# Kernel tuning notes

Measured on AMD Instinct MI355X. Metric: run time of the kernel, lower is better.

## Reference

```python
import jax, jax.numpy as jnp
import numpy as np

N = 51200      # total nodes
G = 256        # graphs in batch
NPG = 200      # nodes per graph
E = 409600     # intra-graph edges
EPG = E // G
F_IN, HID, HEADS, NCLS = 768, 128, 4, 2


def setup_inputs() -> dict:
    key = jax.random.key(0)
    ks = jax.random.split(key, 20)
    x = jax.random.normal(ks[0], (N, F_IN), jnp.float32)
    # edges strictly inside each graph, no self-loops (PyG batching semantics)
    gid = jnp.arange(E, dtype=jnp.int32) // EPG
    sl = jax.random.randint(ks[1], (E,), 0, NPG, dtype=jnp.int32)
    off = jax.random.randint(ks[2], (E,), 1, NPG, dtype=jnp.int32)
    dl = (sl + off) % NPG
    edge_index = jnp.stack([gid * NPG + sl, gid * NPG + dl])
    batch = jnp.arange(N, dtype=jnp.int32) // NPG

    def glorot(k, shape, fan_in):
        return jax.random.normal(k, shape, jnp.float32) * np.float32(1.0 / np.sqrt(fan_in))

    return {
        'x': x, 'edge_index': edge_index, 'batch': batch,
        'W1': glorot(ks[3], (F_IN, HEADS * HID), F_IN),
        'a_src1': glorot(ks[4], (HEADS, HID), HID),
        'a_dst1': glorot(ks[5], (HEADS, HID), HID),
        'b1': jnp.zeros((HEADS * HID,), jnp.float32),
        'W2': glorot(ks[6], (HEADS * HID, HID), HEADS * HID),
        'a_src2': glorot(ks[7], (1, HID), HID),
        'a_dst2': glorot(ks[8], (1, HID), HID),
        'b2': jnp.zeros((HID,), jnp.float32),
        'Wc': glorot(ks[9], (HID, 2), HID),
        'bc': jnp.zeros((2,), jnp.float32),
        'Wf1': glorot(ks[10], (HID, HID), HID),
        'bf1': jnp.zeros((HID,), jnp.float32),
        'Wf2': glorot(ks[11], (HID, NCLS), HID),
        'bf2': jnp.zeros((NCLS,), jnp.float32),
    }


def _segment_softmax(logits, seg, num):
    m = jax.ops.segment_max(logits, seg, num_segments=num)
    e = jnp.exp(logits - m[seg])
    s = jax.ops.segment_sum(e, seg, num_segments=num)
    return e / (s[seg] + 1e-16)


def _gat(x, src, dst, W, a_s, a_d, b, n):
    # PyG GATConv, eval mode (attention dropout off), self-loops already in src/dst
    H, C = a_s.shape
    h = (x @ W).reshape(n, H, C)                       # [n,H,C]
    a_src = (h * a_s).sum(-1)                          # [n,H]
    a_dst = (h * a_d).sum(-1)
    logits = jax.nn.leaky_relu(a_src[src] + a_dst[dst], 0.2)  # [Etot,H]
    alpha = _segment_softmax(logits, dst, n)
    out = jax.ops.segment_sum(h[src] * alpha[:, :, None], dst, num_segments=n)
    return out.reshape(n, H * C) + b


def reference(x, edge_index, batch, W1, a_src1, a_dst1, b1, W2, a_src2, a_dst2, b2,
              Wc, bc, Wf1, bf1, Wf2, bf2):
    src0, dst0 = edge_index[0], edge_index[1]
    loop = jnp.arange(N, dtype=src0.dtype)
    src = jnp.concatenate([src0, loop])
    dst = jnp.concatenate([dst0, loop])

    h1 = jax.nn.relu(_gat(x, src, dst, W1, a_src1, a_dst1, b1, N))     # [N,512]
    h2 = jax.nn.relu(_gat(h1, src, dst, W2, a_src2, a_dst2, b2, N))    # [N,128]

    S = jax.nn.softmax(h2 @ Wc + bc, axis=1)                           # [N,2]

    # aggregate(): per-graph S^T A S via per-edge outer products (A from original edges)
    eg = batch[src0]
    outer = S[src0][:, :, None] * S[dst0][:, None, :]                  # [E,2,2]
    agg = jax.ops.segment_sum(outer, eg, num_segments=G)               # [G,2,2]
    rnorm = jnp.clip(jnp.abs(agg).sum(axis=2, keepdims=True), 1e-5, None)  # F.normalize p=1 dim=1
    nadj = agg / rnorm
    diag = jnp.diagonal(nadj, axis1=1, axis2=2)                        # [G,2]
    aggregate_loss = jnp.mean(jnp.mean((diag - 1.0) ** 2, axis=1))     # MSE vs ones, averaged over graphs

    # subgraph embedding: first row of S_g^T x_g per graph
    sub = jax.ops.segment_sum(S[:, 0:1] * h2, batch, num_segments=G)   # [G,128]

    out = jax.nn.relu(sub @ Wf1 + bf1)                                 # eval: dropout off
    out = out @ Wf2 + bf2                                              # [G,2]
    return out, aggregate_loss
```

## Files before the change

kernel.cpp:

```cpp
#include <hip/hip_runtime.h>
#include <hip/hip_bf16.h>
#include <cstdint>

#define N_NODES 51200
#define N_GRAPH 256
#define NPG     200
#define N_EDGE  409600
#define EPG     1600
#define F_IN    768
#define HID     128
#define HEADS   4
#define HC      512

typedef __attribute__((ext_vector_type(8))) short short8;
typedef __attribute__((ext_vector_type(4))) float floatx4;

constexpr size_t OFF_H1B    = 0;
constexpr size_t OFF_H2B    = OFF_H1B + (size_t)N_NODES * HC * 2;
constexpr size_t OFF_H2F    = OFF_H2B + (size_t)N_NODES * HID * 2;
constexpr size_t OFF_WT1    = OFF_H2F + (size_t)N_NODES * HID * 4;
constexpr size_t OFF_WT2    = OFF_WT1 + (size_t)HC * F_IN * 2;
constexpr size_t OFF_S      = OFF_WT2 + (size_t)HID * HC * 2;
constexpr size_t OFF_AGG    = OFF_S + (size_t)N_NODES * 2 * 4;
constexpr size_t OFF_SUB    = OFF_AGG + (size_t)N_GRAPH * 4 * 4;
constexpr size_t OFF_EORD   = OFF_SUB + (size_t)N_GRAPH * HID * 4;
constexpr size_t OFF_ROWS   = OFF_EORD + (size_t)N_GRAPH * EPG * 2;

__device__ __forceinline__ float leaky(float x) { return x >= 0.0f ? x : 0.2f * x; }

__device__ __forceinline__ unsigned short f2bf(float f) {
    unsigned int u = __float_as_uint(f);
    u += 0x7fffu + ((u >> 16) & 1u);
    return (unsigned short)(u >> 16);
}
__device__ __forceinline__ float bflo(int p) { return __uint_as_float((unsigned)p << 16); }
__device__ __forceinline__ float bfhi(int p) { return __uint_as_float((unsigned)p & 0xffff0000u); }

__device__ __forceinline__ unsigned int cvtpk(float lo, float hi) {
    unsigned int r;
    asm("v_cvt_pk_bf16_f32 %0, %1, %2" : "=v"(r) : "v"(lo), "v"(hi));
    return r;
}

__device__ __forceinline__ void gl_lds16(const void* g, void* l) {
    __builtin_amdgcn_global_load_lds(
        (__attribute__((address_space(1))) void*)(g),
        (__attribute__((address_space(3))) void*)(l),
        16, 0, 0);
}

__global__ __launch_bounds__(256)
void transpose_cvt_kernel(const float* __restrict__ W, short* __restrict__ Wt,
                          int K, int Nn)
{
    int idx = blockIdx.x * 256 + threadIdx.x;
    if (idx >= K * Nn) return;
    int k = idx / Nn, n = idx % Nn;
    Wt[(size_t)n * K + k] = (short)f2bf(W[idx]);
}

__global__ __launch_bounds__(512, 2)
void gemm_xw1_kernel(const float* __restrict__ A, const short* __restrict__ Bt,
                     unsigned short* __restrict__ C, int M, int Nn, int K)
{
    __shared__ __align__(16) float Asm[3][256 * 32];
    __shared__ __align__(16) short Bsm[3][256 * 32];
    const int tid = threadIdx.x;
    const int w = tid >> 6, l = tid & 63;

    const int nwg = gridDim.x;
    int wg = blockIdx.x;
    wg = (wg & 7) * (nwg >> 3) + (wg >> 3);
    const int nbx = Nn >> 8;
    const int m0 = (wg / nbx) * 256;
    const int n0 = (wg % nbx) * 256;
    const int wr = w >> 2, wc = w & 3;

    floatx4 acc[8][4];
#pragma unroll
    for (int i = 0; i < 8; ++i)
#pragma unroll
        for (int j = 0; j < 4; ++j) acc[i][j] = (floatx4)0.0f;

    const short* bgp = Bt + (size_t)(n0 + w * 32 + (l & 15)) * K + ((l >> 4) * 8);
    const float* agp = A + (size_t)(m0 + w * 32 + (l & 7)) * K + ((l >> 3) * 4);
    const int nt = K >> 5;

    int aB[8];
#pragma unroll
    for (int mi = 0; mi < 8; ++mi) {
        const int r = wr * 128 + mi * 16 + (l & 15);
        aB[mi] = (r >> 3) * 256 + (l >> 4) * 64 + (r & 7) * 4;
    }
    const int bB0 = wc * 2048 + l * 8;

#define STAGEX(buf, t) {                                                        \
        const int ko_ = (t) * 32;                                               \
        gl_lds16(agp + ko_,              &Asm[buf][(w * 4 + 0) * 256]);         \
        gl_lds16(agp + 8 * K + ko_,      &Asm[buf][(w * 4 + 1) * 256]);         \
        gl_lds16(agp + 16 * K + ko_,     &Asm[buf][(w * 4 + 2) * 256]);         \
        gl_lds16(agp + 24 * K + ko_,     &Asm[buf][(w * 4 + 3) * 256]);         \
        gl_lds16(bgp + ko_,              &Bsm[buf][w * 1024]);                  \
        gl_lds16(bgp + 16 * K + ko_,     &Bsm[buf][w * 1024 + 512]); }

#define COMPUTEX(buf) {                                                         \
        short8 bfr[4];                                                          \
        _Pragma("unroll")                                                       \
        for (int ni = 0; ni < 4; ++ni)                                          \
            bfr[ni] = *(const short8*)&Bsm[buf][bB0 + ni * 512];                \
        _Pragma("unroll")                                                       \
        for (int mh = 0; mh < 2; ++mh) {                                        \
            short8 af[4];                                                       \
            _Pragma("unroll")                                                   \
            for (int q = 0; q < 4; ++q) {                                       \
                float4 v0 = *(const float4*)&Asm[buf][aB[mh * 4 + q]];          \
                float4 v1 = *(const float4*)&Asm[buf][aB[mh * 4 + q] + 32];     \
                uint4 pk;                                                       \
                pk.x = cvtpk(v0.x, v0.y); pk.y = cvtpk(v0.z, v0.w);             \
                pk.z = cvtpk(v1.x, v1.y); pk.w = cvtpk(v1.z, v1.w);             \
                af[q] = *reinterpret_cast<short8*>(&pk);                        \
            }                                                                   \
            _Pragma("unroll")                                                   \
            for (int q = 0; q < 4; ++q)                                         \
                _Pragma("unroll")                                               \
                for (int ni = 0; ni < 4; ++ni)                                  \
                    acc[mh * 4 + q][ni] = __builtin_amdgcn_mfma_f32_16x16x32_bf16( \
                        af[q], bfr[ni], acc[mh * 4 + q][ni], 0, 0, 0);          \
        } }

    STAGEX(0, 0);
    STAGEX(1, 1);
    asm volatile("s_waitcnt vmcnt(6)" ::: "memory");
    __builtin_amdgcn_s_barrier();

    int cur3 = 0;
    for (int t = 0; t < nt; ++t) {
        int nn3 = cur3 + 2; if (nn3 >= 3) nn3 -= 3;
        if (t + 2 < nt) STAGEX(nn3, t + 2);
        COMPUTEX(cur3);
        if (t + 1 < nt) {
            if (t + 2 < nt) asm volatile("s_waitcnt vmcnt(6) lgkmcnt(0)" ::: "memory");
            else            asm volatile("s_waitcnt vmcnt(0) lgkmcnt(0)" ::: "memory");
            __builtin_amdgcn_s_barrier();
        }
        cur3 += 1; if (cur3 == 3) cur3 = 0;
    }
#undef STAGEX
#undef COMPUTEX

    const int lr = (l >> 4) * 4, lc = l & 15;
#pragma unroll
    for (int mi = 0; mi < 8; ++mi)
#pragma unroll
        for (int ni = 0; ni < 4; ++ni) {
            const size_t base = (size_t)(m0 + wr * 128 + mi * 16 + lr) * Nn
                              + (n0 + wc * 64 + ni * 16 + lc);
#pragma unroll
            for (int rr = 0; rr < 4; ++rr)
                C[base + (size_t)rr * Nn] = f2bf(acc[mi][ni][rr]);
        }
}

__global__ __launch_bounds__(256)
void gemm_bf16_kernel(const short* __restrict__ Ab, const short* __restrict__ Bt,
                      unsigned short* __restrict__ C, int M, int Nn, int K)
{
    __shared__ __align__(16) short Bblob[3][4096];
    __shared__ __align__(16) short Ablob[3][4096];
    const int tid = threadIdx.x;
    const int w = tid >> 6, l = tid & 63;

    const int nwg = gridDim.x;
    int wg = blockIdx.x;
    wg = (wg & 7) * (nwg >> 3) + (wg >> 3);
    const int nbx = Nn >> 7;
    const int m0 = (wg / nbx) * 128;
    const int n0 = (wg % nbx) * 128;
    const int wr = w >> 1, wc = w & 1;
    const int wofs = w * 1024;

    floatx4 acc[4][4];
#pragma unroll
    for (int i = 0; i < 4; ++i)
#pragma unroll
        for (int j = 0; j < 4; ++j) acc[i][j] = (floatx4)0.0f;

    const short* bgp = Bt + (size_t)(n0 + w * 32 + (l & 15)) * K + ((l >> 4) * 8);
    const short* agp = Ab + (size_t)(m0 + w * 32 + (l & 15)) * K + ((l >> 4) * 8);
    const int nt = K >> 5;

    auto compute = [&](int bi) {
        short8 af[4], bfr[4];
#pragma unroll
        for (int mi = 0; mi < 4; ++mi)
            af[mi] = *(const short8*)&Ablob[bi][(wr * 4 + mi) * 512 + l * 8];
#pragma unroll
        for (int ni = 0; ni < 4; ++ni)
            bfr[ni] = *(const short8*)&Bblob[bi][(wc * 4 + ni) * 512 + l * 8];
#pragma unroll
        for (int mi = 0; mi < 4; ++mi)
#pragma unroll
            for (int ni = 0; ni < 4; ++ni)
                acc[mi][ni] = __builtin_amdgcn_mfma_f32_16x16x32_bf16(
                    af[mi], bfr[ni], acc[mi][ni], 0, 0, 0);
    };

    gl_lds16(agp,               &Ablob[0][wofs]);
    gl_lds16(agp + 16 * K,      &Ablob[0][wofs + 512]);
    gl_lds16(bgp,               &Bblob[0][wofs]);
    gl_lds16(bgp + 16 * K,      &Bblob[0][wofs + 512]);
    gl_lds16(agp + 32,          &Ablob[1][wofs]);
    gl_lds16(agp + 16 * K + 32, &Ablob[1][wofs + 512]);
    gl_lds16(bgp + 32,          &Bblob[1][wofs]);
    gl_lds16(bgp + 16 * K + 32, &Bblob[1][wofs + 512]);
    asm volatile("s_waitcnt vmcnt(4)" ::: "memory");
    __builtin_amdgcn_s_barrier();

    int cur3 = 0;
    for (int t = 0; t < nt; ++t) {
        int nn3 = cur3 + 2; if (nn3 >= 3) nn3 -= 3;
        if (t + 2 < nt) {
            const int kk = (t + 2) << 5;
            gl_lds16(agp + kk,          &Ablob[nn3][wofs]);
            gl_lds16(agp + 16 * K + kk, &Ablob[nn3][wofs + 512]);
            gl_lds16(bgp + kk,          &Bblob[nn3][wofs]);
            gl_lds16(bgp + 16 * K + kk, &Bblob[nn3][wofs + 512]);
        }
        compute(cur3);
        if (t + 1 < nt) {
            if (t + 2 < nt) asm volatile("s_waitcnt vmcnt(4) lgkmcnt(0)" ::: "memory");
            else            asm volatile("s_waitcnt vmcnt(0) lgkmcnt(0)" ::: "memory");
            __builtin_amdgcn_s_barrier();
        }
        cur3 += 1; if (cur3 == 3) cur3 = 0;
    }

    const int lr = (l >> 4) * 4, lc = l & 15;
#pragma unroll
    for (int mi = 0; mi < 4; ++mi)
#pragma unroll
        for (int ni = 0; ni < 4; ++ni) {
            const size_t base = (size_t)(m0 + wr * 64 + mi * 16 + lr) * Nn
                              + (n0 + wc * 64 + ni * 16 + lc);
#pragma unroll
            for (int rr = 0; rr < 4; ++rr)
                C[base + (size_t)rr * Nn] = f2bf(acc[mi][ni][rr]);
        }
}

__global__ __launch_bounds__(256)
void csr_kernel(const int* __restrict__ src0, const int* __restrict__ dst0,
                unsigned short* __restrict__ eord, int* __restrict__ rows)
{
    const int g = blockIdx.x, tid = threadIdx.x;
    __shared__ unsigned short s_eraw[EPG];
    __shared__ int s_cnt[NPG];
    __shared__ int s_scan[256];
    __shared__ int s_row[NPG + 1];
    const int gbase = g * NPG;

    if (tid < NPG) s_cnt[tid] = 0;
    for (int j = tid; j < EPG; j += 256) {
        int s = src0[g * EPG + j] - gbase;
        int d = dst0[g * EPG + j] - gbase;
        s_eraw[j] = (unsigned short)(s | (d << 8));
    }
    __syncthreads();
    for (int j = tid; j < EPG; j += 256)
        atomicAdd(&s_cnt[s_eraw[j] >> 8], 1);
    __syncthreads();
    {
        int v = (tid < NPG) ? s_cnt[tid] : 0;
        s_scan[tid] = v;
        __syncthreads();
        for (int off = 1; off < 256; off <<= 1) {
            int u = (tid >= off) ? s_scan[tid - off] : 0;
            __syncthreads();
            s_scan[tid] += u;
            __syncthreads();
        }
        if (tid < NPG) s_row[tid + 1] = s_scan[tid];
        if (tid == 0) s_row[0] = 0;
        __syncthreads();
        if (tid < NPG) s_scan[tid] = s_row[tid];
    }
    __syncthreads();
    for (int j = tid; j < EPG; j += 256) {
        int pk = s_eraw[j];
        int p = atomicAdd(&s_scan[pk >> 8], 1);
        eord[(size_t)g * EPG + p] = (unsigned short)pk;
    }
    if (tid <= NPG) rows[g * (NPG + 1) + tid] = s_row[tid];
}

__global__ __launch_bounds__(512)
void gat1_kernel(const unsigned short* __restrict__ H,
                 const unsigned short* __restrict__ eord, const int* __restrict__ rows,
                 const float* __restrict__ a_s, const float* __restrict__ a_d,
                 const float* __restrict__ b1, unsigned short* __restrict__ out)
{
    const int g = blockIdx.x, h = blockIdx.y;
    __shared__ int   s_feat[NPG * 64];
    __shared__ float s_as[NPG], s_ad[NPG], s_m[NPG], s_inv[NPG];
    __shared__ int   s_row[NPG + 1];
    __shared__ int2  s_wc[EPG];
    const int tid = threadIdx.x, w = tid >> 6, l = tid & 63;
    const int gbase = g * NPG;

    for (int flat = tid; flat < NPG * 16; flat += 512) {
        int row = flat >> 4, q = flat & 15;
        uint4 v = *(const uint4*)(H + (size_t)(gbase + row) * HC + h * HID + q * 8);
        *(uint4*)&s_feat[row * 64 + q * 4] = v;
    }
    for (int j = tid; j < EPG; j += 512)
        s_wc[j].y = eord[(size_t)g * EPG + j];
    if (tid <= NPG) s_row[tid] = rows[g * (NPG + 1) + tid];
    __syncthreads();

    const float2 av = ((const float2*)(a_s + h * HID))[l];
    const float2 dv = ((const float2*)(a_d + h * HID))[l];
    for (int nl = w; nl < NPG; nl += 8) {
        int pk = s_feat[nl * 64 + l];
        float f0 = bflo(pk), f1 = bfhi(pk);
        float ss = f0 * av.x + f1 * av.y;
        float sd = f0 * dv.x + f1 * dv.y;
#pragma unroll
        for (int off = 1; off < 64; off <<= 1) {
            ss += __shfl_xor(ss, off);
            sd += __shfl_xor(sd, off);
        }
        if (l == 0) { s_as[nl] = ss; s_ad[nl] = sd; }
    }
    __syncthreads();

    for (int j = tid; j < EPG; j += 512) {
        int pk = s_wc[j].y;
        s_wc[j].x = __float_as_int(leaky(s_as[pk & 255] + s_ad[pk >> 8]));
    }
    __syncthreads();

    if (tid < NPG) {
        float m = leaky(s_as[tid] + s_ad[tid]);
        int r0 = s_row[tid], r1 = s_row[tid + 1];
        for (int j = r0; j < r1; ++j) m = fmaxf(m, __int_as_float(s_wc[j].x));
        s_m[tid] = m;
    }
    __syncthreads();

    for (int j = tid; j < EPG; j += 512) {
        int2 e = s_wc[j];
        s_wc[j].x = __float_as_int(__expf(__int_as_float(e.x) - s_m[e.y >> 8]));
    }
    __syncthreads();

    if (tid < NPG) {
        float rs = __expf(leaky(s_as[tid] + s_ad[tid]) - s_m[tid]);
        int r0 = s_row[tid], r1 = s_row[tid + 1];
        for (int j = r0; j < r1; ++j) rs += __int_as_float(s_wc[j].x);
        s_inv[tid] = 1.0f / (rs + 1e-16f);
    }
    __syncthreads();

    const float2 bv = ((const float2*)(b1 + h * HID))[l];
    for (int nl = w; nl < NPG; nl += 8) {
        const int r0 = s_row[nl], r1 = s_row[nl + 1];
        const float wself = __expf(leaky(s_as[nl] + s_ad[nl]) - s_m[nl]);
        int spk = s_feat[nl * 64 + l];
        float a0 = wself * bflo(spk), a1 = wself * bfhi(spk);
        float c0 = 0.0f, c1 = 0.0f;
        int j = r0;
        for (; j + 4 <= r1; j += 4) {
            int2 e0 = s_wc[j], e1 = s_wc[j + 1], e2 = s_wc[j + 2], e3 = s_wc[j + 3];
            int p0 = s_feat[(e0.y & 255) * 64 + l];
            int p1 = s_feat[(e1.y & 255) * 64 + l];
            int p2 = s_feat[(e2.y & 255) * 64 + l];
            int p3 = s_feat[(e3.y & 255) * 64 + l];
            float w0 = __int_as_float(e0.x), w1 = __int_as_float(e1.x);
            float w2 = __int_as_float(e2.x), w3 = __int_as_float(e3.x);
            a0 += w0 * bflo(p0); a1 += w0 * bfhi(p0);
            c0 += w1 * bflo(p1); c1 += w1 * bfhi(p1);
            a0 += w2 * bflo(p2); a1 += w2 * bfhi(p2);
            c0 += w3 * bflo(p3); c1 += w3 * bfhi(p3);
        }
        for (; j < r1; ++j) {
            int2 e0 = s_wc[j];
            int p0 = s_feat[(e0.y & 255) * 64 + l];
            float w0 = __int_as_float(e0.x);
            a0 += w0 * bflo(p0); a1 += w0 * bfhi(p0);
        }
        const float inv = s_inv[nl];
        float o0 = (a0 + c0) * inv + bv.x;
        float o1 = (a1 + c1) * inv + bv.y;
        unsigned int st = (unsigned int)f2bf(fmaxf(o0, 0.0f))
                        | ((unsigned int)f2bf(fmaxf(o1, 0.0f)) << 16);
        *(unsigned int*)&out[(size_t)(gbase + nl) * HC + h * HID + 2 * l] = st;
    }
}

__global__ __launch_bounds__(512)
void gat2_kernel(const unsigned short* __restrict__ H,
                 const unsigned short* __restrict__ eord, const int* __restrict__ rows,
                 const float* __restrict__ a_s, const float* __restrict__ a_d,
                 const float* __restrict__ b2, const float* __restrict__ Wc,
                 const float* __restrict__ bc,
                 float* __restrict__ sub, float* __restrict__ agg)
{
    const int g = blockIdx.x;
    __shared__ int   s_feat[NPG * 64];
    __shared__ float s_as[NPG], s_ad[NPG], s_m[NPG], s_inv[NPG];
    __shared__ int   s_row[NPG + 1];
    __shared__ int2  s_wc[EPG];
    __shared__ float2 s_Sv[NPG];
    __shared__ float  s_red[8 * 128];
    __shared__ float  s_aggr[8][4];
    const int tid = threadIdx.x, w = tid >> 6, l = tid & 63;
    const int gbase = g * NPG;

    for (int flat = tid; flat < NPG * 16; flat += 512) {
        int row = flat >> 4, q = flat & 15;
        uint4 v = *(const uint4*)(H + (size_t)(gbase + row) * HID + q * 8);
        *(uint4*)&s_feat[row * 64 + q * 4] = v;
    }
    for (int j = tid; j < EPG; j += 512)
        s_wc[j].y = eord[(size_t)g * EPG + j];
    if (tid <= NPG) s_row[tid] = rows[g * (NPG + 1) + tid];
    __syncthreads();

    const float2 av = ((const float2*)a_s)[l];
    const float2 dv = ((const float2*)a_d)[l];
    for (int nl = w; nl < NPG; nl += 8) {
        int pk = s_feat[nl * 64 + l];
        float f0 = bflo(pk), f1 = bfhi(pk);
        float ss = f0 * av.x + f1 * av.y;
        float sd = f0 * dv.x + f1 * dv.y;
#pragma unroll
        for (int off = 1; off < 64; off <<= 1) {
            ss += __shfl_xor(ss, off);
            sd += __shfl_xor(sd, off);
        }
        if (l == 0) { s_as[nl] = ss; s_ad[nl] = sd; }
    }
    __syncthreads();

    for (int j = tid; j < EPG; j += 512) {
        int pk = s_wc[j].y;
        s_wc[j].x = __float_as_int(leaky(s_as[pk & 255] + s_ad[pk >> 8]));
    }
    __syncthreads();

    if (tid < NPG) {
        float m = leaky(s_as[tid] + s_ad[tid]);
        int r0 = s_row[tid], r1 = s_row[tid + 1];
        for (int j = r0; j < r1; ++j) m = fmaxf(m, __int_as_float(s_wc[j].x));
        s_m[tid] = m;
    }
    __syncthreads();

    for (int j = tid; j < EPG; j += 512) {
        int2 e = s_wc[j];
        s_wc[j].x = __float_as_int(__expf(__int_as_float(e.x) - s_m[e.y >> 8]));
    }
    __syncthreads();

    if (tid < NPG) {
        float rs = __expf(leaky(s_as[tid] + s_ad[tid]) - s_m[tid]);
        int r0 = s_row[tid], r1 = s_row[tid + 1];
        for (int j = r0; j < r1; ++j) rs += __int_as_float(s_wc[j].x);
        s_inv[tid] = 1.0f / (rs + 1e-16f);
    }
    __syncthreads();

    const float2 bv = ((const float2*)b2)[l];
    const float4 wcv = ((const float4*)Wc)[l];
    const float bc0 = bc[0], bc1 = bc[1];
    float accs0 = 0.0f, accs1 = 0.0f;
    for (int nl = w; nl < NPG; nl += 8) {
        const int r0 = s_row[nl], r1 = s_row[nl + 1];
        const float wself = __expf(leaky(s_as[nl] + s_ad[nl]) - s_m[nl]);
        int spk = s_feat[nl * 64 + l];
        float a0 = wself * bflo(spk), a1 = wself * bfhi(spk);
        float c0 = 0.0f, c1 = 0.0f;
        int j = r0;
        for (; j + 4 <= r1; j += 4) {
            int2 e0 = s_wc[j], e1 = s_wc[j + 1], e2 = s_wc[j + 2], e3 = s_wc[j + 3];
            int p0 = s_feat[(e0.y & 255) * 64 + l];
            int p1 = s_feat[(e1.y & 255) * 64 + l];
            int p2 = s_feat[(e2.y & 255) * 64 + l];
            int p3 = s_feat[(e3.y & 255) * 64 + l];
            float w0 = __int_as_float(e0.x), w1 = __int_as_float(e1.x);
            float w2 = __int_as_float(e2.x), w3 = __int_as_float(e3.x);
            a0 += w0 * bflo(p0); a1 += w0 * bfhi(p0);
            c0 += w1 * bflo(p1); c1 += w1 * bfhi(p1);
            a0 += w2 * bflo(p2); a1 += w2 * bfhi(p2);
            c0 += w3 * bflo(p3); c1 += w3 * bfhi(p3);
        }
        for (; j < r1; ++j) {
            int2 e0 = s_wc[j];
            int p0 = s_feat[(e0.y & 255) * 64 + l];
            float w0 = __int_as_float(e0.x);
            a0 += w0 * bflo(p0); a1 += w0 * bfhi(p0);
        }
        const float inv = s_inv[nl];
        float o0 = fmaxf((a0 + c0) * inv + bv.x, 0.0f);
        float o1 = fmaxf((a1 + c1) * inv + bv.y, 0.0f);
        float z0 = o0 * wcv.x + o1 * wcv.z;
        float z1 = o0 * wcv.y + o1 * wcv.w;
#pragma unroll
        for (int off = 1; off < 64; off <<= 1) {
            z0 += __shfl_xor(z0, off);
            z1 += __shfl_xor(z1, off);
        }
        z0 += bc0; z1 += bc1;
        float mm = fmaxf(z0, z1);
        float e0 = __expf(z0 - mm), e1 = __expf(z1 - mm);
        float is = 1.0f / (e0 + e1);
        float s0v = e0 * is, s1v = e1 * is;
        if (l == 0) s_Sv[nl] = make_float2(s0v, s1v);
        accs0 += s0v * o0;
        accs1 += s0v * o1;
    }
    s_red[w * 128 + 2 * l]     = accs0;
    s_red[w * 128 + 2 * l + 1] = accs1;
    __syncthreads();

    float a00 = 0, a01 = 0, a10 = 0, a11 = 0;
    for (int j = tid; j < EPG; j += 512) {
        int pk = s_wc[j].y;
        float2 Ss = s_Sv[pk & 255];
        float2 Sd = s_Sv[pk >> 8];
        a00 += Ss.x * Sd.x; a01 += Ss.x * Sd.y;
        a10 += Ss.y * Sd.x; a11 += Ss.y * Sd.y;
    }
#pragma unroll
    for (int off = 32; off > 0; off >>= 1) {
        a00 += __shfl_down(a00, off); a01 += __shfl_down(a01, off);
        a10 += __shfl_down(a10, off); a11 += __shfl_down(a11, off);
    }
    if (l == 0) { s_aggr[w][0] = a00; s_aggr[w][1] = a01; s_aggr[w][2] = a10; s_aggr[w][3] = a11; }
    __syncthreads();

    if (tid < 128) {
        float s = 0.0f;
#pragma unroll
        for (int w8 = 0; w8 < 8; ++w8) s += s_red[w8 * 128 + tid];
        sub[(size_t)g * HID + tid] = s;
    }
    if (tid < 4) {
        float s = 0.0f;
#pragma unroll
        for (int w8 = 0; w8 < 8; ++w8) s += s_aggr[w8][tid];
        agg[g * 4 + tid] = s;
    }
}

__global__ __launch_bounds__(256)
void loss_kernel(const float* __restrict__ agg, float* __restrict__ out_loss)
{
    int tid = threadIdx.x;
    float a00 = agg[tid*4 + 0], a01 = agg[tid*4 + 1];
    float a10 = agg[tid*4 + 2], a11 = agg[tid*4 + 3];
    float rn0 = fmaxf(fabsf(a00) + fabsf(a01), 1e-5f);
    float rn1 = fmaxf(fabsf(a10) + fabsf(a11), 1e-5f);
    float d0 = a00 / rn0 - 1.0f, d1 = a11 / rn1 - 1.0f;
    float contrib = 0.5f * (d0*d0 + d1*d1);
    for (int off = 32; off > 0; off >>= 1) contrib += __shfl_down(contrib, off);
    __shared__ float sred[4];
    if ((tid & 63) == 0) sred[tid >> 6] = contrib;
    __syncthreads();
    if (tid == 0)
        out_loss[0] = (sred[0] + sred[1] + sred[2] + sred[3]) * (1.0f / N_GRAPH);
}

__global__ __launch_bounds__(128)
void final_kernel(const float* __restrict__ sub, const float* __restrict__ Wf1,
                  const float* __restrict__ bf1, const float* __restrict__ Wf2,
                  const float* __restrict__ bf2, float* __restrict__ out)
{
    __shared__ float s_sub[128];
    __shared__ float s_fc[128];
    const int g = blockIdx.x, t = threadIdx.x;
    s_sub[t] = sub[g*HID + t];
    __syncthreads();
    float acc = bf1[t];
    for (int c = 0; c < 128; ++c)
        acc += s_sub[c] * Wf1[c*128 + t];
    s_fc[t] = fmaxf(acc, 0.0f);
    __syncthreads();
    if (t < 2) {
        float z = bf2[t];
        for (int j = 0; j < 128; ++j) z += s_fc[j] * Wf2[j*2 + t];
        out[g*2 + t] = z;
    }
}

extern "C" void kernel_launch(void* const* d_in, const int* in_sizes, int n_in,
                              void* d_out, int out_size, void* d_ws, size_t ws_size,
                              hipStream_t stream)
{
    const float* x   = (const float*)d_in[0];
    const int*   ei  = (const int*)d_in[1];
    const float* W1  = (const float*)d_in[3];
    const float* as1 = (const float*)d_in[4];
    const float* ad1 = (const float*)d_in[5];
    const float* b1  = (const float*)d_in[6];
    const float* W2  = (const float*)d_in[7];
    const float* as2 = (const float*)d_in[8];
    const float* ad2 = (const float*)d_in[9];
    const float* b2  = (const float*)d_in[10];
    const float* Wc  = (const float*)d_in[11];
    const float* bc  = (const float*)d_in[12];
    const float* Wf1 = (const float*)d_in[13];
    const float* bf1 = (const float*)d_in[14];
    const float* Wf2 = (const float*)d_in[15];
    const float* bf2 = (const float*)d_in[16];
    const int* src0 = ei;
    const int* dst0 = ei + N_EDGE;

    char* ws = (char*)d_ws;
    unsigned short* H1b = (unsigned short*)(ws + OFF_H1B);
    unsigned short* H2b = (unsigned short*)(ws + OFF_H2B);
    short* Wt1   = (short*)(ws + OFF_WT1);
    short* Wt2   = (short*)(ws + OFF_WT2);
    float* aggb  = (float*)(ws + OFF_AGG);
    float* subb  = (float*)(ws + OFF_SUB);
    unsigned short* eord = (unsigned short*)(ws + OFF_EORD);
    int*   rowsb = (int*)(ws + OFF_ROWS);
    float* out   = (float*)d_out;

    transpose_cvt_kernel<<<(F_IN*HC + 255)/256, 256, 0, stream>>>(W1, Wt1, F_IN, HC);
    transpose_cvt_kernel<<<(HC*HID + 255)/256, 256, 0, stream>>>(W2, Wt2, HC, HID);
    csr_kernel<<<N_GRAPH, 256, 0, stream>>>(src0, dst0, eord, rowsb);

    gemm_xw1_kernel<<<(N_NODES/256) * (HC/256), 512, 0, stream>>>(
        x, Wt1, H1b, N_NODES, HC, F_IN);

    gat1_kernel<<<dim3(N_GRAPH, HEADS), 512, 0, stream>>>(
        H1b, eord, rowsb, as1, ad1, b1, H1b);

    gemm_bf16_kernel<<<(N_NODES/128) * (HID/128), 256, 0, stream>>>(
        (const short*)H1b, Wt2, H2b, N_NODES, HID, HC);

    gat2_kernel<<<N_GRAPH, 512, 0, stream>>>(
        H2b, eord, rowsb, as2, ad2, b2, Wc, bc, subb, aggb);

    loss_kernel<<<1, 256, 0, stream>>>(aggb, out + N_GRAPH*2);
    final_kernel<<<N_GRAPH, 128, 0, stream>>>(subb, Wf1, bf1, Wf2, bf2, out);

    (void)in_sizes; (void)n_in; (void)out_size; (void)ws_size;
}
```

Measured before the change: 505.2 us.

## Shrink XW1 GEMM tile, use LDS-direct loads and atomic softmax reductions in GAT

The first GEMM moves from 256x256 tiles with a triple-buffered pipeline to 128x256 tiles with double buffering, using fewer accumulators and less LDS so more workgroups can be resident. Both GAT kernels now stage node features into shared memory with direct global-to-LDS loads instead of register round-trips. The per-destination softmax max and sum are computed with shared-memory atomics (using an order-preserving int encoding for the max) instead of serial per-row loops, which also removes one barrier phase. The trade-offs are shallower latency hiding in the GEMM, more B-matrix reloads, atomic contention, and float atomic sums that are not order-deterministic.

```diff
diff --git a/kernel.cpp b/kernel.cpp
--- a/kernel.cpp
+++ b/kernel.cpp
@@ -36,6 +36,9 @@
 __device__ __forceinline__ float bflo(int p) { return __uint_as_float((unsigned)p << 16); }
 __device__ __forceinline__ float bfhi(int p) { return __uint_as_float((unsigned)p & 0xffff0000u); }
 
+__device__ __forceinline__ int   fmono(float x) { int u = __float_as_int(x); return u ^ ((u >> 31) | 0x80000000); }
+__device__ __forceinline__ float imono(int k)   { int u = k ^ (((~k) >> 31) | 0x80000000); return __int_as_float(u); }
+
 __device__ __forceinline__ unsigned int cvtpk(float lo, float hi) {
     unsigned int r;
     asm("v_cvt_pk_bf16_f32 %0, %1, %2" : "=v"(r) : "v"(lo), "v"(hi));
@@ -59,12 +62,12 @@
     Wt[(size_t)n * K + k] = (short)f2bf(W[idx]);
 }
 
-__global__ __launch_bounds__(512, 2)
+__global__ __launch_bounds__(512, 4)
 void gemm_xw1_kernel(const float* __restrict__ A, const short* __restrict__ Bt,
                      unsigned short* __restrict__ C, int M, int Nn, int K)
 {
-    __shared__ __align__(16) float Asm[3][256 * 32];
-    __shared__ __align__(16) short Bsm[3][256 * 32];
+    __shared__ __align__(16) float Asm[2][128 * 32];
+    __shared__ __align__(16) short Bsm[2][256 * 32];
     const int tid = threadIdx.x;
     const int w = tid >> 6, l = tid & 63;
 
@@ -72,88 +75,75 @@
     int wg = blockIdx.x;
     wg = (wg & 7) * (nwg >> 3) + (wg >> 3);
     const int nbx = Nn >> 8;
-    const int m0 = (wg / nbx) * 256;
+    const int m0 = (wg / nbx) * 128;
     const int n0 = (wg % nbx) * 256;
     const int wr = w >> 2, wc = w & 3;
 
-    floatx4 acc[8][4];
-#pragma unroll
-    for (int i = 0; i < 8; ++i)
+    floatx4 acc[4][4];
+#pragma unroll
+    for (int i = 0; i < 4; ++i)
 #pragma unroll
         for (int j = 0; j < 4; ++j) acc[i][j] = (floatx4)0.0f;
 
     const short* bgp = Bt + (size_t)(n0 + w * 32 + (l & 15)) * K + ((l >> 4) * 8);
-    const float* agp = A + (size_t)(m0 + w * 32 + (l & 7)) * K + ((l >> 3) * 4);
+    const float* agp = A + (size_t)(m0 + w * 16 + (l & 7)) * K + ((l >> 3) * 4);
     const int nt = K >> 5;
 
-    int aB[8];
-#pragma unroll
-    for (int mi = 0; mi < 8; ++mi) {
-        const int r = wr * 128 + mi * 16 + (l & 15);
+    int aB[4];
+#pragma unroll
+    for (int mi = 0; mi < 4; ++mi) {
+        const int r = wr * 64 + mi * 16 + (l & 15);
         aB[mi] = (r >> 3) * 256 + (l >> 4) * 64 + (r & 7) * 4;
     }
     const int bB0 = wc * 2048 + l * 8;
 
 #define STAGEX(buf, t) {                                                        \
         const int ko_ = (t) * 32;                                               \
-        gl_lds16(agp + ko_,              &Asm[buf][(w * 4 + 0) * 256]);         \
-        gl_lds16(agp + 8 * K + ko_,      &Asm[buf][(w * 4 + 1) * 256]);         \
-        gl_lds16(agp + 16 * K + ko_,     &Asm[buf][(w * 4 + 2) * 256]);         \
-        gl_lds16(agp + 24 * K + ko_,     &Asm[buf][(w * 4 + 3) * 256]);         \
+        gl_lds16(agp + ko_,              &Asm[buf][w * 512]);                   \
+        gl_lds16(agp + 8 * K + ko_,      &Asm[buf][w * 512 + 256]);             \
         gl_lds16(bgp + ko_,              &Bsm[buf][w * 1024]);                  \
         gl_lds16(bgp + 16 * K + ko_,     &Bsm[buf][w * 1024 + 512]); }
 
 #define COMPUTEX(buf) {                                                         \
-        short8 bfr[4];                                                          \
+        short8 af[4], bfr[4];                                                   \
+        _Pragma("unroll")                                                       \
+        for (int mi = 0; mi < 4; ++mi) {                                        \
+            float4 v0 = *(const float4*)&Asm[buf][aB[mi]];                      \
+            float4 v1 = *(const float4*)&Asm[buf][aB[mi] + 32];                 \
+            uint4 pk;                                                           \
+            pk.x = cvtpk(v0.x, v0.y); pk.y = cvtpk(v0.z, v0.w);                 \
+            pk.z = cvtpk(v1.x, v1.y); pk.w = cvtpk(v1.z, v1.w);                 \
+            af[mi] = *reinterpret_cast<short8*>(&pk);                           \
+        }                                                                       \
         _Pragma("unroll")                                                       \
         for (int ni = 0; ni < 4; ++ni)                                          \
             bfr[ni] = *(const short8*)&Bsm[buf][bB0 + ni * 512];                \
         _Pragma("unroll")                                                       \
-        for (int mh = 0; mh < 2; ++mh) {                                        \
-            short8 af[4];                                                       \
+        for (int mi = 0; mi < 4; ++mi)                                          \
             _Pragma("unroll")                                                   \
-            for (int q = 0; q < 4; ++q) {                                       \
-                float4 v0 = *(const float4*)&Asm[buf][aB[mh * 4 + q]];          \
-                float4 v1 = *(const float4*)&Asm[buf][aB[mh * 4 + q] + 32];     \
-                uint4 pk;                                                       \
-                pk.x = cvtpk(v0.x, v0.y); pk.y = cvtpk(v0.z, v0.w);             \
-                pk.z = cvtpk(v1.x, v1.y); pk.w = cvtpk(v1.z, v1.w);             \
-                af[q] = *reinterpret_cast<short8*>(&pk);                        \
-            }                                                                   \
-            _Pragma("unroll")                                                   \
-            for (int q = 0; q < 4; ++q)                                         \
-                _Pragma("unroll")                                               \
-                for (int ni = 0; ni < 4; ++ni)                                  \
-                    acc[mh * 4 + q][ni] = __builtin_amdgcn_mfma_f32_16x16x32_bf16( \
-                        af[q], bfr[ni], acc[mh * 4 + q][ni], 0, 0, 0);          \
-        } }
+            for (int ni = 0; ni < 4; ++ni)                                      \
+                acc[mi][ni] = __builtin_amdgcn_mfma_f32_16x16x32_bf16(          \
+                    af[mi], bfr[ni], acc[mi][ni], 0, 0, 0); }
 
     STAGEX(0, 0);
-    STAGEX(1, 1);
-    asm volatile("s_waitcnt vmcnt(6)" ::: "memory");
-    __builtin_amdgcn_s_barrier();
-
-    int cur3 = 0;
+    __syncthreads();
+
+    int cur = 0;
     for (int t = 0; t < nt; ++t) {
-        int nn3 = cur3 + 2; if (nn3 >= 3) nn3 -= 3;
-        if (t + 2 < nt) STAGEX(nn3, t + 2);
-        COMPUTEX(cur3);
-        if (t + 1 < nt) {
-            if (t + 2 < nt) asm volatile("s_waitcnt vmcnt(6) lgkmcnt(0)" ::: "memory");
-            else            asm volatile("s_waitcnt vmcnt(0) lgkmcnt(0)" ::: "memory");
-            __builtin_amdgcn_s_barrier();
-        }
-        cur3 += 1; if (cur3 == 3) cur3 = 0;
+        if (t + 1 < nt) STAGEX(cur ^ 1, t + 1);
+        COMPUTEX(cur);
+        __syncthreads();
+        cur ^= 1;
     }
 #undef STAGEX
 #undef COMPUTEX
 
     const int lr = (l >> 4) * 4, lc = l & 15;
 #pragma unroll
-    for (int mi = 0; mi < 8; ++mi)
+    for (int mi = 0; mi < 4; ++mi)
 #pragma unroll
         for (int ni = 0; ni < 4; ++ni) {
-            const size_t base = (size_t)(m0 + wr * 128 + mi * 16 + lr) * Nn
+            const size_t base = (size_t)(m0 + wr * 64 + mi * 16 + lr) * Nn
                               + (n0 + wc * 64 + ni * 16 + lc);
 #pragma unroll
             for (int rr = 0; rr < 4; ++rr)
@@ -301,16 +291,21 @@
 {
     const int g = blockIdx.x, h = blockIdx.y;
     __shared__ int   s_feat[NPG * 64];
-    __shared__ float s_as[NPG], s_ad[NPG], s_m[NPG], s_inv[NPG];
+    __shared__ float s_as[NPG], s_ad[NPG], s_m[NPG], s_sum[NPG];
+    __shared__ int   s_mi[NPG];
     __shared__ int   s_row[NPG + 1];
     __shared__ int2  s_wc[EPG];
     const int tid = threadIdx.x, w = tid >> 6, l = tid & 63;
     const int gbase = g * NPG;
 
-    for (int flat = tid; flat < NPG * 16; flat += 512) {
-        int row = flat >> 4, q = flat & 15;
-        uint4 v = *(const uint4*)(H + (size_t)(gbase + row) * HC + h * HID + q * 8);
-        *(uint4*)&s_feat[row * 64 + q * 4] = v;
+    for (int c = 0; c < 7; ++c) {
+        const int base = c * 512 + w * 64;
+        if (base < NPG * 16) {
+            const int flat = base + l;
+            const int row = flat >> 4, q = flat & 15;
+            gl_lds16(H + (size_t)(gbase + row) * HC + h * HID + q * 8,
+                     &s_feat[base * 4]);
+        }
     }
     for (int j = tid; j < EPG; j += 512)
         s_wc[j].y = eord[(size_t)g * EPG + j];
@@ -329,35 +324,33 @@
             ss += __shfl_xor(ss, off);
             sd += __shfl_xor(sd, off);
         }
-        if (l == 0) { s_as[nl] = ss; s_ad[nl] = sd; }
+        if (l == 0) {
+            s_as[nl] = ss; s_ad[nl] = sd;
+            s_mi[nl] = fmono(leaky(ss + sd));
+        }
     }
     __syncthreads();
 
     for (int j = tid; j < EPG; j += 512) {
         int pk = s_wc[j].y;
-        s_wc[j].x = __float_as_int(leaky(s_as[pk & 255] + s_ad[pk >> 8]));
+        float lg = leaky(s_as[pk & 255] + s_ad[pk >> 8]);
+        s_wc[j].x = __float_as_int(lg);
+        atomicMax(&s_mi[pk >> 8], fmono(lg));
     }
     __syncthreads();
 
     if (tid < NPG) {
-        float m = leaky(s_as[tid] + s_ad[tid]);
-        int r0 = s_row[tid], r1 = s_row[tid + 1];
-        for (int j = r0; j < r1; ++j) m = fmaxf(m, __int_as_float(s_wc[j].x));
+        float m = imono(s_mi[tid]);
         s_m[tid] = m;
+        s_sum[tid] = __expf(leaky(s_as[tid] + s_ad[tid]) - m);
     }
     __syncthreads();
 
     for (int j = tid; j < EPG; j += 512) {
         int2 e = s_wc[j];
-        s_wc[j].x = __float_as_int(__expf(__int_as_float(e.x) - s_m[e.y >> 8]));
-    }
-    __syncthreads();
-
-    if (tid < NPG) {
-        float rs = __expf(leaky(s_as[tid] + s_ad[tid]) - s_m[tid]);
-        int r0 = s_row[tid], r1 = s_row[tid + 1];
-        for (int j = r0; j < r1; ++j) rs += __int_as_float(s_wc[j].x);
-        s_inv[tid] = 1.0f / (rs + 1e-16f);
+        float ev = __expf(__int_as_float(e.x) - s_m[e.y >> 8]);
+        s_wc[j].x = __float_as_int(ev);
+        atomicAdd(&s_sum[e.y >> 8], ev);
     }
     __syncthreads();
 
@@ -388,7 +381,7 @@
             float w0 = __int_as_float(e0.x);
             a0 += w0 * bflo(p0); a1 += w0 * bfhi(p0);
         }
-        const float inv = s_inv[nl];
+        const float inv = 1.0f / (s_sum[nl] + 1e-16f);
         float o0 = (a0 + c0) * inv + bv.x;
         float o1 = (a1 + c1) * inv + bv.y;
         unsigned int st = (unsigned int)f2bf(fmaxf(o0, 0.0f))
@@ -407,7 +400,8 @@
 {
     const int g = blockIdx.x;
     __shared__ int   s_feat[NPG * 64];
-    __shared__ float s_as[NPG], s_ad[NPG], s_m[NPG], s_inv[NPG];
+    __shared__ float s_as[NPG], s_ad[NPG], s_m[NPG], s_sum[NPG];
+    __shared__ int   s_mi[NPG];
     __shared__ int   s_row[NPG + 1];
     __shared__ int2  s_wc[EPG];
     __shared__ float2 s_Sv[NPG];
@@ -416,10 +410,11 @@
     const int tid = threadIdx.x, w = tid >> 6, l = tid & 63;
     const int gbase = g * NPG;
 
-    for (int flat = tid; flat < NPG * 16; flat += 512) {
-        int row = flat >> 4, q = flat & 15;
-        uint4 v = *(const uint4*)(H + (size_t)(gbase + row) * HID + q * 8);
-        *(uint4*)&s_feat[row * 64 + q * 4] = v;
+    for (int c = 0; c < 7; ++c) {
+        const int base = c * 512 + w * 64;
+        if (base < NPG * 16)
+            gl_lds16(H + (size_t)gbase * HID + (size_t)(base + l) * 8,
+                     &s_feat[base * 4]);
     }
     for (int j = tid; j < EPG; j += 512)
         s_wc[j].y = eord[(size_t)g * EPG + j];
@@ -438,35 +433,33 @@
             ss += __shfl_xor(ss, off);
             sd += __shfl_xor(sd, off);
         }
-        if (l == 0) { s_as[nl] = ss; s_ad[nl] = sd; }
+        if (l == 0) {
+            s_as[nl] = ss; s_ad[nl] = sd;
+            s_mi[nl] = fmono(leaky(ss + sd));
+        }
     }
     __syncthreads();
 
     for (int j = tid; j < EPG; j += 512) {
         int pk = s_wc[j].y;
-        s_wc[j].x = __float_as_int(leaky(s_as[pk & 255] + s_ad[pk >> 8]));
+        float lg = leaky(s_as[pk & 255] + s_ad[pk >> 8]);
+        s_wc[j].x = __float_as_int(lg);
+        atomicMax(&s_mi[pk >> 8], fmono(lg));
     }
     __syncthreads();
 
     if (tid < NPG) {
-        float m = leaky(s_as[tid] + s_ad[tid]);
-        int r0 = s_row[tid], r1 = s_row[tid + 1];
-        for (int j = r0; j < r1; ++j) m = fmaxf(m, __int_as_float(s_wc[j].x));
+        float m = imono(s_mi[tid]);
         s_m[tid] = m;
+        s_sum[tid] = __expf(leaky(s_as[tid] + s_ad[tid]) - m);
     }
     __syncthreads();
 
     for (int j = tid; j < EPG; j += 512) {
         int2 e = s_wc[j];
-        s_wc[j].x = __float_as_int(__expf(__int_as_float(e.x) - s_m[e.y >> 8]));
-    }
-    __syncthreads();
-
-    if (tid < NPG) {
-        float rs = __expf(leaky(s_as[tid] + s_ad[tid]) - s_m[tid]);
-        int r0 = s_row[tid], r1 = s_row[tid + 1];
-        for (int j = r0; j < r1; ++j) rs += __int_as_float(s_wc[j].x);
-        s_inv[tid] = 1.0f / (rs + 1e-16f);
+        float ev = __expf(__int_as_float(e.x) - s_m[e.y >> 8]);
+        s_wc[j].x = __float_as_int(ev);
+        atomicAdd(&s_sum[e.y >> 8], ev);
     }
     __syncthreads();
 
@@ -500,7 +493,7 @@
             float w0 = __int_as_float(e0.x);
             a0 += w0 * bflo(p0); a1 += w0 * bfhi(p0);
         }
-        const float inv = s_inv[nl];
+        const float inv = 1.0f / (s_sum[nl] + 1e-16f);
         float o0 = fmaxf((a0 + c0) * inv + bv.x, 0.0f);
         float o1 = fmaxf((a1 + c1) * inv + bv.y, 0.0f);
         float z0 = o0 * wcv.x + o1 * wcv.z;
@@ -631,7 +624,7 @@
     transpose_cvt_kernel<<<(HC*HID + 255)/256, 256, 0, stream>>>(W2, Wt2, HC, HID);
     csr_kernel<<<N_GRAPH, 256, 0, stream>>>(src0, dst0, eord, rowsb);
 
-    gemm_xw1_kernel<<<(N_NODES/256) * (HC/256), 512, 0, stream>>>(
+    gemm_xw1_kernel<<<(N_NODES/128) * (HC/256), 512, 0, stream>>>(
         x, Wt1, H1b, N_NODES, HC, F_IN);
 
     gat1_kernel<<<dim3(N_GRAPH, HEADS), 512, 0, stream>>>(
```

New measurement: 509.0 us. About the same (+0.7%).
